# Optimization experiments

Measured on AMD Instinct MI355X. Metric: run time of the kernel, lower is better.

Reference implementation:

```python
import jax, jax.numpy as jnp
import numpy as np

HEADS = 8
DIM_HEAD = 32
SCALE = DIM_HEAD ** (-0.5)


def setup_inputs() -> dict:
    key = jax.random.key(0)
    k1, k2, k3, k4 = jax.random.split(key, 4)
    x = jax.random.normal(k1, (16, 256, 64, 64), dtype=jnp.float32)
    # conv 1x1 weights stored as [out_ch, in_ch]
    w_qkv = jax.random.normal(k2, (3 * HEADS * DIM_HEAD, 256), dtype=jnp.float32) * 0.05
    w_out = jax.random.normal(k3, (256, HEADS * DIM_HEAD), dtype=jnp.float32) * 0.05
    b_out = jax.random.normal(k4, (256,), dtype=jnp.float32) * 0.05
    return {"x": x, "w_qkv": w_qkv, "w_out": w_out, "b_out": b_out}


def reference(x, w_qkv, w_out, b_out):
    b, c, h, w = x.shape
    n = h * w
    # 1x1 conv (no bias) == channel matmul
    qkv = jnp.einsum('bchw,oc->bohw', x, w_qkv)            # [b, 3*H*D, h, w]
    qkv = qkv.reshape(b, 3, HEADS, DIM_HEAD, n)            # chunk then 'b (h c) xy'
    q, k, v = qkv[:, 0], qkv[:, 1], qkv[:, 2]              # [b, H, D, n]
    q = jax.nn.softmax(q, axis=-2) * SCALE                 # softmax over channel dim d
    k = jax.nn.softmax(k, axis=-1)                         # softmax over spatial n
    context = jnp.einsum('bhdn,bhen->bhde', k, v)          # [b, H, D, D]
    out = jnp.einsum('bhde,bhdn->bhen', context, q)        # [b, H, D, n]
    out = out.reshape(b, HEADS * DIM_HEAD, h, w)
    # 1x1 conv with bias
    return jnp.einsum('bchw,oc->bohw', out, w_out) + b_out[None, :, None, None]
```

## Files before the change

kernel.cpp:

```cpp
#include <hip/hip_runtime.h>
#include <cstddef>
#include <cstdint>

#define NN 4096
#define CIN 256
#define CQKV 768
#define NBATCH 16
#define QSCALE 0.17677669529663687f

typedef short s16x8 __attribute__((ext_vector_type(8)));
typedef float f32x4 __attribute__((ext_vector_type(4)));

__device__ __forceinline__ float bf2f(unsigned short u) {
    unsigned int x = ((unsigned int)u) << 16;
    return __builtin_bit_cast(float, x);
}
__device__ __forceinline__ unsigned short f2bf(float f) {
    unsigned int u = __builtin_bit_cast(unsigned int, f);
    return (unsigned short)((u + 0x7fffu + ((u >> 16) & 1u)) >> 16);
}
__device__ __forceinline__ void glds16(const void* gsrc, void* lds) {
    __builtin_amdgcn_global_load_lds(
        (const __attribute__((address_space(1))) unsigned int*)gsrc,
        (__attribute__((address_space(3))) unsigned int*)lds,
        16, 0, 0);
}

__global__ __launch_bounds__(256)
void xpose(const float* __restrict__ x, unsigned short* __restrict__ xT)
{
    const int b = blockIdx.z;
    const int n0 = blockIdx.x * 64, c0 = blockIdx.y * 64;
    __shared__ float xs[64][65];
    const int t = threadIdx.x;
    const float* xb = x + (size_t)b * CIN * NN;
#pragma unroll
    for (int p = 0; p < 4; ++p) {
        const int row = p * 16 + (t >> 4);
        const int col = (t & 15) * 4;
        const float4 v = *reinterpret_cast<const float4*>(
            &xb[(size_t)(c0 + row) * NN + n0 + col]);
        xs[col + 0][row] = v.x; xs[col + 1][row] = v.y;
        xs[col + 2][row] = v.z; xs[col + 3][row] = v.w;
    }
    __syncthreads();
    const int n = t >> 2, cch = (t & 3) * 16;
    unsigned short arr[16];
#pragma unroll
    for (int e = 0; e < 16; ++e) arr[e] = f2bf(xs[n][cch + e]);
    unsigned short* dst = xT + ((size_t)b * NN + n0 + n) * 256 + c0 + cch;
    *reinterpret_cast<s16x8*>(&dst[0]) = *reinterpret_cast<s16x8*>(&arr[0]);
    *reinterpret_cast<s16x8*>(&dst[8]) = *reinterpret_cast<s16x8*>(&arr[8]);
}

__global__ __launch_bounds__(256)
void wcvt(const float* __restrict__ w, unsigned short* __restrict__ wb)
{
    const int i = (blockIdx.x * 256 + threadIdx.x) * 4;
    const float4 v = *reinterpret_cast<const float4*>(&w[i]);
    unsigned short a[4] = { f2bf(v.x), f2bf(v.y), f2bf(v.z), f2bf(v.w) };
    *reinterpret_cast<ushort2*>(&wb[i])     = *reinterpret_cast<ushort2*>(&a[0]);
    *reinterpret_cast<ushort2*>(&wb[i + 2]) = *reinterpret_cast<ushort2*>(&a[2]);
}

__device__ __forceinline__ void gemm_pipe3(const unsigned short* __restrict__ Ab,
                                           const unsigned short* __restrict__ Bb,
                                           int m0, int n0, char* smem,
                                           f32x4 (&acc)[4][4])
{
    const int t = threadIdx.x;
    const int lane = t & 63, w = t >> 6;
    const int lr = lane & 15, lq = lane >> 4;
    const int wr = (w >> 1) * 64, wc = (w & 1) * 64;
    const int ch0 = (w * 2 + 0) * 64 + lane;
    const int ch1 = (w * 2 + 1) * 64 + lane;
    const int r0 = ch0 >> 2, c0s = (ch0 & 3) ^ ((r0 >> 1) & 3);
    const int r1 = ch1 >> 2, c1s = (ch1 & 3) ^ ((r1 >> 1) & 3);
    char* Abuf = smem;
    char* Bbuf = smem + 24576;

#define STG_H(h)                                                               \
  { char* ab = Abuf + ((h) % 3) * 8192;                                        \
    char* bb = Bbuf + ((h) % 3) * 8192;                                        \
    glds16(Ab + (size_t)(m0 + r0) * 256 + (h) * 32 + c0s * 8, ab + (w*2+0)*1024); \
    glds16(Ab + (size_t)(m0 + r1) * 256 + (h) * 32 + c1s * 8, ab + (w*2+1)*1024); \
    glds16(Bb + (size_t)(n0 + r0) * 256 + (h) * 32 + c0s * 8, bb + (w*2+0)*1024); \
    glds16(Bb + (size_t)(n0 + r1) * 256 + (h) * 32 + c1s * 8, bb + (w*2+1)*1024); }

#define CMP_H(h)                                                               \
  { char* ab = Abuf + ((h) % 3) * 8192;                                        \
    char* bb = Bbuf + ((h) % 3) * 8192;                                        \
    s16x8 af[4], bfr[4];                                                       \
    _Pragma("unroll") for (int m = 0; m < 4; ++m) {                            \
        const int row = wr + m * 16 + lr;                                      \
        af[m] = *(const s16x8*)(ab + row * 64 + ((lq ^ ((row >> 1) & 3)) << 4)); } \
    _Pragma("unroll") for (int n = 0; n < 4; ++n) {                            \
        const int col = wc + n * 16 + lr;                                      \
        bfr[n] = *(const s16x8*)(bb + col * 64 + ((lq ^ ((col >> 1) & 3)) << 4)); } \
    __builtin_amdgcn_s_setprio(1);                                             \
    _Pragma("unroll") for (int m = 0; m < 4; ++m)                              \
    _Pragma("unroll") for (int n = 0; n < 4; ++n)                              \
        acc[m][n] = __builtin_amdgcn_mfma_f32_16x16x32_bf16(af[m], bfr[n],     \
                                                            acc[m][n], 0, 0, 0); \
    __builtin_amdgcn_s_setprio(0); }

    STG_H(0); STG_H(1);
#pragma unroll
    for (int i = 0; i < 8; ++i) {
        if (i < 7) asm volatile("s_waitcnt vmcnt(4)" ::: "memory");
        else       asm volatile("s_waitcnt vmcnt(0)" ::: "memory");
        __builtin_amdgcn_s_barrier();
        __builtin_amdgcn_sched_barrier(0);
        if (i < 6) STG_H(i + 2);
        CMP_H(i);
    }
#undef STG_H
#undef CMP_H
}

__global__ __launch_bounds__(256, 3)
void qkv_fused(const unsigned short* __restrict__ wb,
               const unsigned short* __restrict__ xT,
               unsigned short* __restrict__ qT,
               float* __restrict__ ctx_part,
               float* __restrict__ z_part)
{
    __shared__ __align__(16) char smem[49152];
    const int nt = blockIdx.x;
    const int ty = blockIdx.y;
    const int b  = blockIdx.z;
    const int t = threadIdx.x;
    const int lane = t & 63, w = t >> 6;
    const int lr = lane & 15, lq = lane >> 4;
    const int wr = (w >> 1) * 64, wc = (w & 1) * 64;
    const int n0 = nt * 128;

    if (ty < 2) {
        const int m0 = ty * 128;
        const unsigned short* Bb = xT + (size_t)b * NN * 256;
        f32x4 acc[4][4] = {};
        gemm_pipe3(wb, Bb, m0, n0, smem, acc);

        __syncthreads();
        unsigned short (*qs)[136] = (unsigned short (*)[136])smem;
#pragma unroll
        for (int n = 0; n < 4; ++n) {
            const int col = wc + n * 16 + lr;
#pragma unroll
            for (int hp = 0; hp < 2; ++hp) {
                float mx = -1e30f;
#pragma unroll
                for (int u = 0; u < 2; ++u)
#pragma unroll
                    for (int r = 0; r < 4; ++r)
                        mx = fmaxf(mx, acc[hp * 2 + u][n][r]);
                mx = fmaxf(mx, __shfl_xor(mx, 16));
                mx = fmaxf(mx, __shfl_xor(mx, 32));
                float er[2][4];
                float s = 0.f;
#pragma unroll
                for (int u = 0; u < 2; ++u)
#pragma unroll
                    for (int r = 0; r < 4; ++r) {
                        er[u][r] = __expf(acc[hp * 2 + u][n][r] - mx);
                        s += er[u][r];
                    }
                s += __shfl_xor(s, 16);
                s += __shfl_xor(s, 32);
                const float inv = QSCALE / s;
#pragma unroll
                for (int u = 0; u < 2; ++u) {
                    ushort4 pk;
                    pk.x = f2bf(er[u][0] * inv);
                    pk.y = f2bf(er[u][1] * inv);
                    pk.z = f2bf(er[u][2] * inv);
                    pk.w = f2bf(er[u][3] * inv);
                    *(ushort4*)&qs[col][wr + (hp * 2 + u) * 16 + lq * 4] = pk;
                }
            }
        }
        __syncthreads();
        const int nl = t >> 1, half = t & 1;
        const unsigned short* src = &qs[nl][half * 64];
        unsigned short* dst = qT + ((size_t)b * NN + n0 + nl) * 256 + m0 + half * 64;
#pragma unroll
        for (int i = 0; i < 8; ++i)
            *(s16x8*)(dst + i * 8) = *(const s16x8*)(src + i * 8);
    } else {
        const int g = ty - 2;
        const unsigned short* An = xT + ((size_t)b * NN + (size_t)n0) * 256;

        f32x4 acc[4][4] = {};
        gemm_pipe3(An, wb, 0, 256 + g * 128, smem, acc);

        unsigned int ekpk[4][4][2];
        float zl[4] = {0.f, 0.f, 0.f, 0.f};
#pragma unroll
        for (int m = 0; m < 4; ++m)
#pragma unroll
            for (int nn = 0; nn < 4; ++nn) {
                const unsigned short u0 = f2bf(__expf(acc[m][nn][0]));
                const unsigned short u1 = f2bf(__expf(acc[m][nn][1]));
                const unsigned short u2 = f2bf(__expf(acc[m][nn][2]));
                const unsigned short u3 = f2bf(__expf(acc[m][nn][3]));
                zl[nn] += bf2f(u0) + bf2f(u1) + bf2f(u2) + bf2f(u3);
                ekpk[m][nn][0] = (unsigned int)u0 | ((unsigned int)u1 << 16);
                ekpk[m][nn][1] = (unsigned int)u2 | ((unsigned int)u3 << 16);
            }
#pragma unroll
        for (int nn = 0; nn < 4; ++nn) {
            zl[nn] += __shfl_xor(zl[nn], 16);
            zl[nn] += __shfl_xor(zl[nn], 32);
        }
        const float zv = (lq == 0) ? zl[0] : (lq == 1) ? zl[1] : (lq == 2) ? zl[2] : zl[3];
        z_part[((((size_t)(b * 32 + nt)) * 2 + g) * 2 + (w >> 1)) * 128 + wc + lane] = zv;

#pragma unroll
        for (int m = 0; m < 4; ++m)
#pragma unroll
            for (int nn = 0; nn < 4; ++nn) acc[m][nn] = (f32x4){0.f, 0.f, 0.f, 0.f};
        gemm_pipe3(An, wb, 0, 512 + g * 128, smem, acc);

        __syncthreads();
        f32x4 cacc[2][2] = {};
#pragma unroll
        for (int p = 0; p < 2; ++p) {
            if ((w >> 1) == p) {
#pragma unroll
                for (int m = 0; m < 4; ++m)
#pragma unroll
                    for (int nn = 0; nn < 4; ++nn) {
                        const int col = wc + nn * 16 + lr;
                        const int swz = (col & 7) << 4;
                        const int rowb = (m * 16 + lq * 4) * 2;
                        *(unsigned int*)(smem + ((col * 128 + rowb) ^ swz))
                            = ekpk[m][nn][0];
                        *(unsigned int*)(smem + ((col * 128 + rowb + 4) ^ swz))
                            = ekpk[m][nn][1];
                        const unsigned int vp0 = (unsigned int)f2bf(acc[m][nn][0])
                            | ((unsigned int)f2bf(acc[m][nn][1]) << 16);
                        const unsigned int vp1 = (unsigned int)f2bf(acc[m][nn][2])
                            | ((unsigned int)f2bf(acc[m][nn][3]) << 16);
                        *(unsigned int*)(smem + 16384 +
                            ((col * 128 + rowb) ^ swz)) = vp0;
                        *(unsigned int*)(smem + 16384 +
                            ((col * 128 + rowb + 4) ^ swz)) = vp1;
                    }
            }
            __syncthreads();
#pragma unroll
            for (int ks2 = 0; ks2 < 2; ++ks2) {
                s16x8 afk[2], bfv[2];
#pragma unroll
                for (int dt = 0; dt < 2; ++dt) {
                    const int drow = w * 32 + dt * 16 + lr;
                    afk[dt] = *(const s16x8*)(smem + drow * 128 +
                        ((((ks2 * 4 + lq) ^ (drow & 7))) << 4));
                }
#pragma unroll
                for (int et = 0; et < 2; ++et) {
                    const int erow = w * 32 + et * 16 + lr;
                    bfv[et] = *(const s16x8*)(smem + 16384 + erow * 128 +
                        ((((ks2 * 4 + lq) ^ (erow & 7))) << 4));
                }
#pragma unroll
                for (int dt = 0; dt < 2; ++dt)
#pragma unroll
                    for (int et = 0; et < 2; ++et)
                        cacc[dt][et] = __builtin_amdgcn_mfma_f32_16x16x32_bf16(
                            afk[dt], bfv[et], cacc[dt][et], 0, 0, 0);
            }
            __syncthreads();
        }
        float* cp = ctx_part + ((((size_t)(b * 32 + nt)) * 2 + g) * 4 + w) * 1024;
#pragma unroll
        for (int dt = 0; dt < 2; ++dt)
#pragma unroll
            for (int et = 0; et < 2; ++et)
#pragma unroll
                for (int r = 0; r < 4; ++r)
                    cp[(dt * 16 + lq * 4 + r) * 32 + et * 16 + lr] = cacc[dt][et][r];
    }
}

__global__ __launch_bounds__(256)
void make_m(const float* __restrict__ ctx_part, const float* __restrict__ z_part,
            const float* __restrict__ w_out, unsigned short* __restrict__ Mmat)
{
    const int h = blockIdx.x, b = blockIdx.y;
    const int g = h >> 2, hh = h & 3;
    const int t = threadIdx.x;
    __shared__ float ctx[32][33];
    __shared__ float zinv[32];

    for (int c = t; c < 1024; c += 256) {
        float s = 0.f;
#pragma unroll 8
        for (int nt = 0; nt < 32; ++nt)
            s += ctx_part[((((size_t)(b * 32 + nt)) * 2 + g) * 4 + hh) * 1024 + c];
        ctx[c >> 5][c & 31] = s;
    }
    if (t < 32) {
        float z = 0.f;
#pragma unroll 8
        for (int nt = 0; nt < 32; ++nt) {
            const size_t base = (((size_t)(b * 32 + nt)) * 2 + g) * 2;
            z += z_part[(base + 0) * 128 + hh * 32 + t];
            z += z_part[(base + 1) * 128 + hh * 32 + t];
        }
        zinv[t] = 1.f / z;
    }
    __syncthreads();

    const int o = t;
    float wrow[32];
#pragma unroll
    for (int e = 0; e < 32; ++e)
        wrow[e] = w_out[(size_t)o * 256 + h * 32 + e];
#pragma unroll 4
    for (int d = 0; d < 32; ++d) {
        float s = 0.f;
#pragma unroll
        for (int e = 0; e < 32; ++e)
            s = fmaf(wrow[e], ctx[d][e], s);
        Mmat[((size_t)b * 256 + o) * 256 + h * 32 + d] = f2bf(s * zinv[d]);
    }
}

__global__ __launch_bounds__(256, 3)
void gemm_out(const unsigned short* __restrict__ Mmat,
              const unsigned short* __restrict__ qT,
              float* __restrict__ out, const float* __restrict__ bias)
{
    __shared__ __align__(16) char smem[49152];
    const int bz = blockIdx.z;
    const int m0 = blockIdx.y * 128, n0 = blockIdx.x * 128;
    const unsigned short* Ab = Mmat + (size_t)bz * 256 * 256;
    const unsigned short* Bb = qT + (size_t)bz * NN * 256;

    f32x4 acc[4][4] = {};
    gemm_pipe3(Ab, Bb, m0, n0, smem, acc);

    const int t = threadIdx.x;
    const int lane = t & 63, w = t >> 6;
    const int lr = lane & 15, lq = lane >> 4;
    const int wc = (w & 1) * 64;

    __syncthreads();
    float* Yb = out + (size_t)bz * CIN * NN;
#pragma unroll
    for (int hf = 0; hf < 2; ++hf) {
        if ((w >> 1) == hf) {
#pragma unroll
            for (int m = 0; m < 4; ++m)
#pragma unroll
                for (int r = 0; r < 4; ++r) {
                    const int rl = m * 16 + lq * 4 + r;
                    const float bv = bias[m0 + hf * 64 + rl];
                    const int rb = rl * 512;
                    const int xs = (rl & 7) << 4;
#pragma unroll
                    for (int n = 0; n < 4; ++n) {
                        const int col = wc + n * 16 + lr;
                        *(float*)(smem + rb + ((col * 4) ^ xs)) = acc[m][n][r] + bv;
                    }
                }
        }
        __syncthreads();
#pragma unroll
        for (int p = 0; p < 4; ++p) {
            const int rl = p * 16 + (t >> 4);
            const int rb = rl * 512;
            const int xs = (rl & 7) << 4;
            const int cb = (t & 15) * 32;
            const float4 v0 = *(const float4*)(smem + rb + ((cb + 0) ^ xs));
            const float4 v1 = *(const float4*)(smem + rb + ((cb + 16) ^ xs));
            float* dst = Yb + (size_t)(m0 + hf * 64 + rl) * NN + n0 + (t & 15) * 8;
            *(float4*)dst = v0;
            *(float4*)(dst + 4) = v1;
        }
        __syncthreads();
    }
}

extern "C" void kernel_launch(void* const* d_in, const int* in_sizes, int n_in,
                              void* d_out, int out_size, void* d_ws, size_t ws_size,
                              hipStream_t stream)
{
    const float* x     = (const float*)d_in[0];
    const float* w_qkv = (const float*)d_in[1];
    const float* w_out = (const float*)d_in[2];
    const float* b_out = (const float*)d_in[3];
    float* out = (float*)d_out;

    char* ws = (char*)d_ws;
    size_t off = 0;
    unsigned short* xT  = (unsigned short*)(ws + off);  off += (size_t)NBATCH * NN * CIN * 2;
    unsigned short* qT  = (unsigned short*)(ws + off);  off += (size_t)NBATCH * NN * CIN * 2;
    float* ctx_part     = (float*)(ws + off);           off += (size_t)NBATCH * 32 * 2 * 4 * 1024 * 4;
    float* z_part       = (float*)(ws + off);           off += (size_t)NBATCH * 32 * 2 * 2 * 128 * 4;
    unsigned short* Mmat= (unsigned short*)(ws + off);  off += (size_t)NBATCH * 256 * 256 * 2;
    unsigned short* wb  = (unsigned short*)(ws + off);  off += (size_t)CQKV * CIN * 2;

    xpose<<<dim3(NN / 64, CIN / 64, NBATCH), 256, 0, stream>>>(x, xT);
    wcvt<<<dim3(CQKV * CIN / 1024), 256, 0, stream>>>(w_qkv, wb);

    qkv_fused<<<dim3(32, 4, NBATCH), 256, 0, stream>>>(wb, xT, qT, ctx_part, z_part);

    make_m<<<dim3(8, NBATCH), 256, 0, stream>>>(ctx_part, z_part, w_out, Mmat);

    gemm_out<<<dim3(32, 2, NBATCH), 256, 0, stream>>>(Mmat, qT, out, b_out);
}
```

Baseline: 105.8 us.

## Restructure QKV kernel into 256-wide asymmetric tiles with interleaved K/V weights

The QKV projection kernel now uses three block types per spatial tile instead of four. One block computes all 256 query channels with an 8x4 MFMA tile per wave, and two blocks each compute a fused 256-column K|V tile for a head group. This removes the second sequential GEMM pass in the K/V blocks and the duplicated loads of the x slab. A new weight-convert kernel reorders w_qkv rows so each group's K and V rows are contiguous. The cost is more LDS (72KB) and more accumulator registers, so occupancy drops to 2 blocks per CU, and there are fewer blocks overall.

```diff
diff --git a/kernel.cpp b/kernel.cpp
--- a/kernel.cpp
+++ b/kernel.cpp
@@ -54,13 +54,285 @@
 }
 
 __global__ __launch_bounds__(256)
-void wcvt(const float* __restrict__ w, unsigned short* __restrict__ wb)
+void wcvt2(const float* __restrict__ w, unsigned short* __restrict__ wb2)
 {
     const int i = (blockIdx.x * 256 + threadIdx.x) * 4;
-    const float4 v = *reinterpret_cast<const float4*>(&w[i]);
+    const int row = i >> 8, col = i & 255;
+    int orow;
+    if (row < 256) orow = row;
+    else {
+        const int g = (row - 256) >> 8;
+        const int within = (row - 256) & 255;
+        const int half = within >> 7;
+        const int idx = within & 127;
+        orow = 256 + half * 256 + g * 128 + idx;
+    }
+    const float4 v = *reinterpret_cast<const float4*>(&w[(size_t)orow * 256 + col]);
     unsigned short a[4] = { f2bf(v.x), f2bf(v.y), f2bf(v.z), f2bf(v.w) };
-    *reinterpret_cast<ushort2*>(&wb[i])     = *reinterpret_cast<ushort2*>(&a[0]);
-    *reinterpret_cast<ushort2*>(&wb[i + 2]) = *reinterpret_cast<ushort2*>(&a[2]);
+    *reinterpret_cast<ushort2*>(&wb2[i])     = *reinterpret_cast<ushort2*>(&a[0]);
+    *reinterpret_cast<ushort2*>(&wb2[i + 2]) = *reinterpret_cast<ushort2*>(&a[2]);
+}
+
+template<int MF, int NF>
+__device__ __forceinline__ void gemm_asym(const unsigned short* __restrict__ Ab,
+                                          const unsigned short* __restrict__ Bb,
+                                          char* __restrict__ smem,
+                                          f32x4 (&acc)[MF][NF])
+{
+    constexpr int AW = MF / 2;
+    constexpr int BW = NF / 2;
+    constexpr int ASTG = MF * 2048;
+    constexpr int BSTG = NF * 2048;
+    const int t = threadIdx.x;
+    const int lane = t & 63, w = t >> 6;
+    const int lr = lane & 15, lq = lane >> 4;
+    const int wr = (w >> 1) * (MF * 16), wc = (w & 1) * (NF * 16);
+    char* Abuf = smem;
+    char* Bbuf = smem + 3 * ASTG;
+
+#define STG_H(h)                                                               \
+  { char* ab = Abuf + ((h) % 3) * ASTG;                                        \
+    char* bb = Bbuf + ((h) % 3) * BSTG;                                        \
+    _Pragma("unroll") for (int j = 0; j < AW; ++j) {                           \
+        const int ch = (w * AW + j) * 64 + lane;                               \
+        const int row = ch >> 2, c = (ch & 3) ^ ((row >> 1) & 3);              \
+        glds16(Ab + (size_t)row * 256 + (h) * 32 + c * 8,                      \
+               ab + (w * AW + j) * 1024); }                                    \
+    _Pragma("unroll") for (int j = 0; j < BW; ++j) {                           \
+        const int ch = (w * BW + j) * 64 + lane;                               \
+        const int row = ch >> 2, c = (ch & 3) ^ ((row >> 1) & 3);              \
+        glds16(Bb + (size_t)row * 256 + (h) * 32 + c * 8,                      \
+               bb + (w * BW + j) * 1024); } }
+
+#define CMP_H(h)                                                               \
+  { char* ab = Abuf + ((h) % 3) * ASTG;                                        \
+    char* bb = Bbuf + ((h) % 3) * BSTG;                                        \
+    s16x8 af[MF], bfr[NF];                                                     \
+    _Pragma("unroll") for (int m = 0; m < MF; ++m) {                           \
+        const int row = wr + m * 16 + lr;                                      \
+        af[m] = *(const s16x8*)(ab + row * 64 + ((lq ^ ((row >> 1) & 3)) << 4)); } \
+    _Pragma("unroll") for (int nn = 0; nn < NF; ++nn) {                        \
+        const int col = wc + nn * 16 + lr;                                     \
+        bfr[nn] = *(const s16x8*)(bb + col * 64 + ((lq ^ ((col >> 1) & 3)) << 4)); } \
+    __builtin_amdgcn_s_setprio(1);                                             \
+    _Pragma("unroll") for (int m = 0; m < MF; ++m)                             \
+    _Pragma("unroll") for (int nn = 0; nn < NF; ++nn)                          \
+        acc[m][nn] = __builtin_amdgcn_mfma_f32_16x16x32_bf16(af[m], bfr[nn],   \
+                                                             acc[m][nn], 0, 0, 0); \
+    __builtin_amdgcn_s_setprio(0); }
+
+    STG_H(0); STG_H(1);
+#pragma unroll
+    for (int i = 0; i < 8; ++i) {
+        if (i < 7) asm volatile("s_waitcnt vmcnt(6)" ::: "memory");
+        else       asm volatile("s_waitcnt vmcnt(0)" ::: "memory");
+        __builtin_amdgcn_s_barrier();
+        __builtin_amdgcn_sched_barrier(0);
+        if (i < 6) STG_H(i + 2);
+        CMP_H(i);
+    }
+#undef STG_H
+#undef CMP_H
+}
+
+__global__ __launch_bounds__(256, 2)
+void qkv_fused(const unsigned short* __restrict__ wb2,
+               const unsigned short* __restrict__ xT,
+               unsigned short* __restrict__ qT,
+               float* __restrict__ ctx_part,
+               float* __restrict__ z_part)
+{
+    __shared__ __align__(16) char smem[73728];
+    const int nt = blockIdx.x;
+    const int ty = blockIdx.y;
+    const int b  = blockIdx.z;
+    const int t = threadIdx.x;
+    const int lane = t & 63, w = t >> 6;
+    const int lr = lane & 15, lq = lane >> 4;
+    const int n0 = nt * 128;
+    const unsigned short* xslab = xT + ((size_t)b * NN + n0) * 256;
+
+    if (ty == 0) {
+        const int wr = (w >> 1) * 128, wc = (w & 1) * 64;
+        f32x4 acc[8][4] = {};
+        gemm_asym<8, 4>(wb2, xslab, smem, acc);
+
+        __syncthreads();
+#pragma unroll
+        for (int nn = 0; nn < 4; ++nn) {
+            const int col = wc + nn * 16 + lr;
+            const int swz = (col & 7) << 4;
+#pragma unroll
+            for (int hp = 0; hp < 4; ++hp) {
+                float mx = -1e30f;
+#pragma unroll
+                for (int u = 0; u < 2; ++u)
+#pragma unroll
+                    for (int r = 0; r < 4; ++r)
+                        mx = fmaxf(mx, acc[hp * 2 + u][nn][r]);
+                mx = fmaxf(mx, __shfl_xor(mx, 16));
+                mx = fmaxf(mx, __shfl_xor(mx, 32));
+                float er[2][4];
+                float s = 0.f;
+#pragma unroll
+                for (int u = 0; u < 2; ++u)
+#pragma unroll
+                    for (int r = 0; r < 4; ++r) {
+                        er[u][r] = __expf(acc[hp * 2 + u][nn][r] - mx);
+                        s += er[u][r];
+                    }
+                s += __shfl_xor(s, 16);
+                s += __shfl_xor(s, 32);
+                const float inv = QSCALE / s;
+#pragma unroll
+                for (int u = 0; u < 2; ++u) {
+                    ushort4 pk;
+                    pk.x = f2bf(er[u][0] * inv);
+                    pk.y = f2bf(er[u][1] * inv);
+                    pk.z = f2bf(er[u][2] * inv);
+                    pk.w = f2bf(er[u][3] * inv);
+                    const int cbyte = (wr + hp * 32 + u * 16 + lq * 4) * 2;
+                    *(ushort4*)(smem + ((col * 512 + cbyte) ^ swz)) = pk;
+                }
+            }
+        }
+        __syncthreads();
+        const int nl = t >> 1, half = t & 1;
+        unsigned short* dst = qT + ((size_t)b * NN + n0 + nl) * 256 + half * 128;
+        const int rswz = (nl & 7) << 4;
+#pragma unroll
+        for (int i = 0; i < 16; ++i) {
+            const int boff = (nl * 512 + half * 256 + i * 16) ^ rswz;
+            *(s16x8*)(dst + i * 8) = *(const s16x8*)(smem + boff);
+        }
+    } else {
+        const int g = ty - 1;
+        f32x4 acc[4][8] = {};
+        gemm_asym<4, 8>(xslab, wb2 + (size_t)(256 + g * 256) * 256, smem, acc);
+
+        if ((w & 1) == 0) {
+            float zl[8];
+#pragma unroll
+            for (int nn = 0; nn < 8; ++nn) zl[nn] = 0.f;
+#pragma unroll
+            for (int m = 0; m < 4; ++m)
+#pragma unroll
+                for (int nn = 0; nn < 8; ++nn)
+#pragma unroll
+                    for (int r = 0; r < 4; ++r) {
+                        const float e = bf2f(f2bf(__expf(acc[m][nn][r])));
+                        acc[m][nn][r] = e;
+                        zl[nn] += e;
+                    }
+#pragma unroll
+            for (int nn = 0; nn < 8; ++nn) {
+                zl[nn] += __shfl_xor(zl[nn], 16);
+                zl[nn] += __shfl_xor(zl[nn], 32);
+            }
+            float* zp = z_part + ((((size_t)(b * 32 + nt)) * 2 + g) * 2 + (w >> 1)) * 128;
+            zp[lane]      = zl[lq];
+            zp[64 + lane] = zl[4 + lq];
+        }
+
+        __syncthreads();
+        f32x4 cacc[2][2] = {};
+#pragma unroll
+        for (int p = 0; p < 2; ++p) {
+            if ((w >> 1) == p) {
+                char* base = (w & 1) ? (smem + 16384) : smem;
+#pragma unroll
+                for (int m = 0; m < 4; ++m)
+#pragma unroll
+                    for (int nn = 0; nn < 8; ++nn) {
+                        const int col = nn * 16 + lr;
+                        const int swz = (col & 7) << 4;
+                        const int rowb = (m * 16 + lq * 4) * 2;
+                        const unsigned int p0 = (unsigned int)f2bf(acc[m][nn][0])
+                            | ((unsigned int)f2bf(acc[m][nn][1]) << 16);
+                        const unsigned int p1 = (unsigned int)f2bf(acc[m][nn][2])
+                            | ((unsigned int)f2bf(acc[m][nn][3]) << 16);
+                        *(unsigned int*)(base + ((col * 128 + rowb) ^ swz))     = p0;
+                        *(unsigned int*)(base + ((col * 128 + rowb + 4) ^ swz)) = p1;
+                    }
+            }
+            __syncthreads();
+#pragma unroll
+            for (int ks2 = 0; ks2 < 2; ++ks2) {
+                s16x8 afk[2], bfv[2];
+#pragma unroll
+                for (int dt = 0; dt < 2; ++dt) {
+                    const int drow = w * 32 + dt * 16 + lr;
+                    afk[dt] = *(const s16x8*)(smem + drow * 128 +
+                        ((((ks2 * 4 + lq) ^ (drow & 7))) << 4));
+                }
+#pragma unroll
+                for (int et = 0; et < 2; ++et) {
+                    const int erow = w * 32 + et * 16 + lr;
+                    bfv[et] = *(const s16x8*)(smem + 16384 + erow * 128 +
+                        ((((ks2 * 4 + lq) ^ (erow & 7))) << 4));
+                }
+#pragma unroll
+                for (int dt = 0; dt < 2; ++dt)
+#pragma unroll
+                    for (int et = 0; et < 2; ++et)
+                        cacc[dt][et] = __builtin_amdgcn_mfma_f32_16x16x32_bf16(
+                            afk[dt], bfv[et], cacc[dt][et], 0, 0, 0);
+            }
+            __syncthreads();
+        }
+        float* cp = ctx_part + ((((size_t)(b * 32 + nt)) * 2 + g) * 4 + w) * 1024;
+#pragma unroll
+        for (int dt = 0; dt < 2; ++dt)
+#pragma unroll
+            for (int et = 0; et < 2; ++et)
+#pragma unroll
+                for (int r = 0; r < 4; ++r)
+                    cp[(dt * 16 + lq * 4 + r) * 32 + et * 16 + lr] = cacc[dt][et][r];
+    }
+}
+
+__global__ __launch_bounds__(256)
+void make_m(const float* __restrict__ ctx_part, const float* __restrict__ z_part,
+            const float* __restrict__ w_out, unsigned short* __restrict__ Mmat)
+{
+    const int h = blockIdx.x, b = blockIdx.y;
+    const int g = h >> 2, hh = h & 3;
+    const int t = threadIdx.x;
+    __shared__ float ctx[32][33];
+    __shared__ float zinv[32];
+
+    for (int c = t; c < 1024; c += 256) {
+        float s = 0.f;
+#pragma unroll 8
+        for (int nt = 0; nt < 32; ++nt)
+            s += ctx_part[((((size_t)(b * 32 + nt)) * 2 + g) * 4 + hh) * 1024 + c];
+        ctx[c >> 5][c & 31] = s;
+    }
+    if (t < 32) {
+        float z = 0.f;
+#pragma unroll 8
+        for (int nt = 0; nt < 32; ++nt) {
+            const size_t base = (((size_t)(b * 32 + nt)) * 2 + g) * 2;
+            z += z_part[(base + 0) * 128 + hh * 32 + t];
+            z += z_part[(base + 1) * 128 + hh * 32 + t];
+        }
+        zinv[t] = 1.f / z;
+    }
+    __syncthreads();
+
+    const int o = t;
+    float wrow[32];
+#pragma unroll
+    for (int e = 0; e < 32; ++e)
+        wrow[e] = w_out[(size_t)o * 256 + h * 32 + e];
+#pragma unroll 4
+    for (int d = 0; d < 32; ++d) {
+        float s = 0.f;
+#pragma unroll
+        for (int e = 0; e < 32; ++e)
+            s = fmaf(wrow[e], ctx[d][e], s);
+        Mmat[((size_t)b * 256 + o) * 256 + h * 32 + d] = f2bf(s * zinv[d]);
+    }
 }
 
 __device__ __forceinline__ void gemm_pipe3(const unsigned short* __restrict__ Ab,
@@ -119,215 +391,6 @@
 }
 
 __global__ __launch_bounds__(256, 3)
-void qkv_fused(const unsigned short* __restrict__ wb,
-               const unsigned short* __restrict__ xT,
-               unsigned short* __restrict__ qT,
-               float* __restrict__ ctx_part,
-               float* __restrict__ z_part)
-{
-    __shared__ __align__(16) char smem[49152];
-    const int nt = blockIdx.x;
-    const int ty = blockIdx.y;
-    const int b  = blockIdx.z;
-    const int t = threadIdx.x;
-    const int lane = t & 63, w = t >> 6;
-    const int lr = lane & 15, lq = lane >> 4;
-    const int wr = (w >> 1) * 64, wc = (w & 1) * 64;
-    const int n0 = nt * 128;
-
-    if (ty < 2) {
-        const int m0 = ty * 128;
-        const unsigned short* Bb = xT + (size_t)b * NN * 256;
-        f32x4 acc[4][4] = {};
-        gemm_pipe3(wb, Bb, m0, n0, smem, acc);
-
-        __syncthreads();
-        unsigned short (*qs)[136] = (unsigned short (*)[136])smem;
-#pragma unroll
-        for (int n = 0; n < 4; ++n) {
-            const int col = wc + n * 16 + lr;
-#pragma unroll
-            for (int hp = 0; hp < 2; ++hp) {
-                float mx = -1e30f;
-#pragma unroll
-                for (int u = 0; u < 2; ++u)
-#pragma unroll
-                    for (int r = 0; r < 4; ++r)
-                        mx = fmaxf(mx, acc[hp * 2 + u][n][r]);
-                mx = fmaxf(mx, __shfl_xor(mx, 16));
-                mx = fmaxf(mx, __shfl_xor(mx, 32));
-                float er[2][4];
-                float s = 0.f;
-#pragma unroll
-                for (int u = 0; u < 2; ++u)
-#pragma unroll
-                    for (int r = 0; r < 4; ++r) {
-                        er[u][r] = __expf(acc[hp * 2 + u][n][r] - mx);
-                        s += er[u][r];
-                    }
-                s += __shfl_xor(s, 16);
-                s += __shfl_xor(s, 32);
-                const float inv = QSCALE / s;
-#pragma unroll
-                for (int u = 0; u < 2; ++u) {
-                    ushort4 pk;
-                    pk.x = f2bf(er[u][0] * inv);
-                    pk.y = f2bf(er[u][1] * inv);
-                    pk.z = f2bf(er[u][2] * inv);
-                    pk.w = f2bf(er[u][3] * inv);
-                    *(ushort4*)&qs[col][wr + (hp * 2 + u) * 16 + lq * 4] = pk;
-                }
-            }
-        }
-        __syncthreads();
-        const int nl = t >> 1, half = t & 1;
-        const unsigned short* src = &qs[nl][half * 64];
-        unsigned short* dst = qT + ((size_t)b * NN + n0 + nl) * 256 + m0 + half * 64;
-#pragma unroll
-        for (int i = 0; i < 8; ++i)
-            *(s16x8*)(dst + i * 8) = *(const s16x8*)(src + i * 8);
-    } else {
-        const int g = ty - 2;
-        const unsigned short* An = xT + ((size_t)b * NN + (size_t)n0) * 256;
-
-        f32x4 acc[4][4] = {};
-        gemm_pipe3(An, wb, 0, 256 + g * 128, smem, acc);
-
-        unsigned int ekpk[4][4][2];
-        float zl[4] = {0.f, 0.f, 0.f, 0.f};
-#pragma unroll
-        for (int m = 0; m < 4; ++m)
-#pragma unroll
-            for (int nn = 0; nn < 4; ++nn) {
-                const unsigned short u0 = f2bf(__expf(acc[m][nn][0]));
-                const unsigned short u1 = f2bf(__expf(acc[m][nn][1]));
-                const unsigned short u2 = f2bf(__expf(acc[m][nn][2]));
-                const unsigned short u3 = f2bf(__expf(acc[m][nn][3]));
-                zl[nn] += bf2f(u0) + bf2f(u1) + bf2f(u2) + bf2f(u3);
-                ekpk[m][nn][0] = (unsigned int)u0 | ((unsigned int)u1 << 16);
-                ekpk[m][nn][1] = (unsigned int)u2 | ((unsigned int)u3 << 16);
-            }
-#pragma unroll
-        for (int nn = 0; nn < 4; ++nn) {
-            zl[nn] += __shfl_xor(zl[nn], 16);
-            zl[nn] += __shfl_xor(zl[nn], 32);
-        }
-        const float zv = (lq == 0) ? zl[0] : (lq == 1) ? zl[1] : (lq == 2) ? zl[2] : zl[3];
-        z_part[((((size_t)(b * 32 + nt)) * 2 + g) * 2 + (w >> 1)) * 128 + wc + lane] = zv;
-
-#pragma unroll
-        for (int m = 0; m < 4; ++m)
-#pragma unroll
-            for (int nn = 0; nn < 4; ++nn) acc[m][nn] = (f32x4){0.f, 0.f, 0.f, 0.f};
-        gemm_pipe3(An, wb, 0, 512 + g * 128, smem, acc);
-
-        __syncthreads();
-        f32x4 cacc[2][2] = {};
-#pragma unroll
-        for (int p = 0; p < 2; ++p) {
-            if ((w >> 1) == p) {
-#pragma unroll
-                for (int m = 0; m < 4; ++m)
-#pragma unroll
-                    for (int nn = 0; nn < 4; ++nn) {
-                        const int col = wc + nn * 16 + lr;
-                        const int swz = (col & 7) << 4;
-                        const int rowb = (m * 16 + lq * 4) * 2;
-                        *(unsigned int*)(smem + ((col * 128 + rowb) ^ swz))
-                            = ekpk[m][nn][0];
-                        *(unsigned int*)(smem + ((col * 128 + rowb + 4) ^ swz))
-                            = ekpk[m][nn][1];
-                        const unsigned int vp0 = (unsigned int)f2bf(acc[m][nn][0])
-                            | ((unsigned int)f2bf(acc[m][nn][1]) << 16);
-                        const unsigned int vp1 = (unsigned int)f2bf(acc[m][nn][2])
-                            | ((unsigned int)f2bf(acc[m][nn][3]) << 16);
-                        *(unsigned int*)(smem + 16384 +
-                            ((col * 128 + rowb) ^ swz)) = vp0;
-                        *(unsigned int*)(smem + 16384 +
-                            ((col * 128 + rowb + 4) ^ swz)) = vp1;
-                    }
-            }
-            __syncthreads();
-#pragma unroll
-            for (int ks2 = 0; ks2 < 2; ++ks2) {
-                s16x8 afk[2], bfv[2];
-#pragma unroll
-                for (int dt = 0; dt < 2; ++dt) {
-                    const int drow = w * 32 + dt * 16 + lr;
-                    afk[dt] = *(const s16x8*)(smem + drow * 128 +
-                        ((((ks2 * 4 + lq) ^ (drow & 7))) << 4));
-                }
-#pragma unroll
-                for (int et = 0; et < 2; ++et) {
-                    const int erow = w * 32 + et * 16 + lr;
-                    bfv[et] = *(const s16x8*)(smem + 16384 + erow * 128 +
-                        ((((ks2 * 4 + lq) ^ (erow & 7))) << 4));
-                }
-#pragma unroll
-                for (int dt = 0; dt < 2; ++dt)
-#pragma unroll
-                    for (int et = 0; et < 2; ++et)
-                        cacc[dt][et] = __builtin_amdgcn_mfma_f32_16x16x32_bf16(
-                            afk[dt], bfv[et], cacc[dt][et], 0, 0, 0);
-            }
-            __syncthreads();
-        }
-        float* cp = ctx_part + ((((size_t)(b * 32 + nt)) * 2 + g) * 4 + w) * 1024;
-#pragma unroll
-        for (int dt = 0; dt < 2; ++dt)
-#pragma unroll
-            for (int et = 0; et < 2; ++et)
-#pragma unroll
-                for (int r = 0; r < 4; ++r)
-                    cp[(dt * 16 + lq * 4 + r) * 32 + et * 16 + lr] = cacc[dt][et][r];
-    }
-}
-
-__global__ __launch_bounds__(256)
-void make_m(const float* __restrict__ ctx_part, const float* __restrict__ z_part,
-            const float* __restrict__ w_out, unsigned short* __restrict__ Mmat)
-{
-    const int h = blockIdx.x, b = blockIdx.y;
-    const int g = h >> 2, hh = h & 3;
-    const int t = threadIdx.x;
-    __shared__ float ctx[32][33];
-    __shared__ float zinv[32];
-
-    for (int c = t; c < 1024; c += 256) {
-        float s = 0.f;
-#pragma unroll 8
-        for (int nt = 0; nt < 32; ++nt)
-            s += ctx_part[((((size_t)(b * 32 + nt)) * 2 + g) * 4 + hh) * 1024 + c];
-        ctx[c >> 5][c & 31] = s;
-    }
-    if (t < 32) {
-        float z = 0.f;
-#pragma unroll 8
-        for (int nt = 0; nt < 32; ++nt) {
-            const size_t base = (((size_t)(b * 32 + nt)) * 2 + g) * 2;
-            z += z_part[(base + 0) * 128 + hh * 32 + t];
-            z += z_part[(base + 1) * 128 + hh * 32 + t];
-        }
-        zinv[t] = 1.f / z;
-    }
-    __syncthreads();
-
-    const int o = t;
-    float wrow[32];
-#pragma unroll
-    for (int e = 0; e < 32; ++e)
-        wrow[e] = w_out[(size_t)o * 256 + h * 32 + e];
-#pragma unroll 4
-    for (int d = 0; d < 32; ++d) {
-        float s = 0.f;
-#pragma unroll
-        for (int e = 0; e < 32; ++e)
-            s = fmaf(wrow[e], ctx[d][e], s);
-        Mmat[((size_t)b * 256 + o) * 256 + h * 32 + d] = f2bf(s * zinv[d]);
-    }
-}
-
-__global__ __launch_bounds__(256, 3)
 void gemm_out(const unsigned short* __restrict__ Mmat,
               const unsigned short* __restrict__ qT,
               float* __restrict__ out, const float* __restrict__ bias)
@@ -400,12 +463,12 @@
     float* ctx_part     = (float*)(ws + off);           off += (size_t)NBATCH * 32 * 2 * 4 * 1024 * 4;
     float* z_part       = (float*)(ws + off);           off += (size_t)NBATCH * 32 * 2 * 2 * 128 * 4;
     unsigned short* Mmat= (unsigned short*)(ws + off);  off += (size_t)NBATCH * 256 * 256 * 2;
-    unsigned short* wb  = (unsigned short*)(ws + off);  off += (size_t)CQKV * CIN * 2;
+    unsigned short* wb2 = (unsigned short*)(ws + off);  off += (size_t)CQKV * CIN * 2;
 
     xpose<<<dim3(NN / 64, CIN / 64, NBATCH), 256, 0, stream>>>(x, xT);
-    wcvt<<<dim3(CQKV * CIN / 1024), 256, 0, stream>>>(w_qkv, wb);
-
-    qkv_fused<<<dim3(32, 4, NBATCH), 256, 0, stream>>>(wb, xT, qT, ctx_part, z_part);
+    wcvt2<<<dim3(CQKV * CIN / 1024), 256, 0, stream>>>(w_qkv, wb2);
+
+    qkv_fused<<<dim3(32, 3, NBATCH), 256, 0, stream>>>(wb2, xT, qT, ctx_part, z_part);
 
     make_m<<<dim3(8, NBATCH), 256, 0, stream>>>(ctx_part, z_part, w_out, Mmat);
 
```

Result: slower. 110.6 us (+4.6%).
